# Kernel optimization log

Measured on AMD Instinct MI355X. Metric: run time of the kernel, lower is better.

Reference implementation:

```python
import jax, jax.numpy as jnp
import numpy as np

B, T, D, H, DK, DV, FF = 4, 1024, 1024, 16, 64, 64, 4096


def setup_inputs() -> dict:
    key = jax.random.key(0)
    ks = jax.random.split(key, 16)
    sc = 0.02  # init scale (original uses uninitialized torch.empty; use small randn)
    n = lambda k, shape: jax.random.normal(k, shape, jnp.float32) * sc
    return dict(
        x=jax.random.normal(ks[0], (B, T, D), jnp.float32),
        y=jax.random.normal(ks[1], (B, T, D), jnp.float32),
        Wq1=n(ks[2], (H, D, DK)), Wk1=n(ks[3], (H, D, DK)),
        Wv1=n(ks[4], (H, D, DV)), Wo1=n(ks[5], (D, D)),
        Wq2=n(ks[6], (H, D, DK)), Wk2=n(ks[7], (H, D, DK)),
        Wv2=n(ks[8], (H, D, DV)), Wo2=n(ks[9], (D, D)),
        W_in=n(ks[10], (FF, D)), b_in=jnp.zeros((FF,), jnp.float32),
        W_out=n(ks[11], (D, FF)), b_out=jnp.zeros((D,), jnp.float32),
    )


def _mha(q, k, v, Wq, Wk, Wv, Wo):
    # per-head projections: (B,T,D) x (H,D,dk) -> (B,H,T,dk)
    WQ = jnp.einsum('btd,hdk->bhtk', q, Wq)
    WK = jnp.einsum('bsd,hdk->bhsk', k, Wk)
    WV = jnp.einsum('bsd,hdv->bhsv', v, Wv)
    scores = jnp.einsum('bhtk,bhsk->bhts', WQ, WK) / jnp.sqrt(jnp.float32(DK))
    # NOTE: original code softmaxes over dim=2 (the QUERY axis), kept faithfully
    attn = jax.nn.softmax(scores, axis=2)
    partial = jnp.einsum('bhts,bhsv->bhtv', attn, WV)
    partial = partial.transpose(0, 2, 1, 3).reshape(q.shape[0], q.shape[1], -1)  # (B,T,H*dv)
    return partial @ Wo


def _sub_norm(o):
    mean = o.mean(-1, keepdims=True)
    std = o.std(-1, ddof=1, keepdims=True)  # torch.std default is unbiased
    return o - mean - std  # faithful: subtract (not divide by) std


def reference(x, y, Wq1, Wk1, Wv1, Wo1, Wq2, Wk2, Wv2, Wo2, W_in, b_in, W_out, b_out):
    out1 = _sub_norm(_mha(y, y, y, Wq1, Wk1, Wv1, Wo1) + y)
    out2 = _sub_norm(_mha(y, x, x, Wq2, Wk2, Wv2, Wo2) + out1)
    ff = jax.nn.relu(y @ W_in.T + b_in) @ W_out.T + b_out  # FFN applied to y, as in source
    return _sub_norm(ff + out2)
```

## Files before the change

kernel.cpp:

```cpp
#include <hip/hip_runtime.h>


typedef unsigned short u16;
typedef __bf16 bf16x8 __attribute__((ext_vector_type(8)));
typedef float f32x4 __attribute__((ext_vector_type(4)));

__device__ __forceinline__ u16 f2bf(float f) {
    unsigned int u = __float_as_uint(f);
    u += 0x7fffu + ((u >> 16) & 1u);
    return (u16)(u >> 16);
}
__device__ __forceinline__ float bf2f(u16 b) {
    return __uint_as_float(((unsigned int)b) << 16);
}

typedef __attribute__((address_space(1))) const void* as1cv;
typedef __attribute__((address_space(3))) void* as3v;
__device__ __forceinline__ void gl_lds16(const void* g, void* l) {
    __builtin_amdgcn_global_load_lds((as1cv)g, (as3v)l, 16, 0, 0);
}


__global__ __launch_bounds__(256) void convert_f2b_k(const float* __restrict__ in, u16* __restrict__ out) {
    long i = (long)blockIdx.x * 256 + threadIdx.x;
    float4 v = reinterpret_cast<const float4*>(in)[i];
    ushort4 o;
    o.x = f2bf(v.x); o.y = f2bf(v.y); o.z = f2bf(v.z); o.w = f2bf(v.w);
    reinterpret_cast<ushort4*>(out)[i] = o;
}

__global__ __launch_bounds__(256) void pack_perm_t(const float* __restrict__ in, u16* __restrict__ out,
                                                   int Q, int R) {
    __shared__ float tile[64][65];
    int p = blockIdx.z;
    int r0 = blockIdx.x * 64, q0 = blockIdx.y * 64;
    int tx = threadIdx.x & 63, ty = threadIdx.x >> 6;
    const float* inp = in + ((long)p * Q + q0) * R + r0;
    #pragma unroll
    for (int i = 0; i < 64; i += 4)
        tile[ty + i][tx] = inp[(long)(ty + i) * R + tx];
    __syncthreads();
    u16* outp = out + ((long)p * R + r0) * Q + q0;
    #pragma unroll
    for (int i = 0; i < 64; i += 4)
        outp[(long)(ty + i) * Q + tx] = f2bf(tile[tx][ty + i]);
}

__global__ __launch_bounds__(256) void transpose_k(const u16* __restrict__ in, long ld_in, long z_in,
                                                   u16* __restrict__ out, long ld_out, long z_out) {
    __shared__ u16 tile[64][66];
    const u16* inz = in + (long)blockIdx.z * z_in;
    u16* outz = out + (long)blockIdx.z * z_out;
    int r0 = blockIdx.y * 64;
    int c0 = blockIdx.x * 64;
    int tx = threadIdx.x & 63, ty = threadIdx.x >> 6;
    #pragma unroll
    for (int i = 0; i < 64; i += 4)
        tile[ty + i][tx] = inz[(long)(r0 + ty + i) * ld_in + c0 + tx];
    __syncthreads();
    #pragma unroll
    for (int i = 0; i < 64; i += 4)
        outz[(long)(c0 + ty + i) * ld_out + r0 + tx] = tile[tx][ty + i];
}

template<int BM, int BN, int BK, int WM, int WN, int OUT_BF16, int EPI, int SWZ, int KS>
__global__ __launch_bounds__(256) void gemm_k(
    const u16* __restrict__ A, long lda, long a_zin, long a_zout,
    const u16* __restrict__ B, long ldb, long b_zin, long b_zout,
    void* __restrict__ Cv, long ldc, long c_zin, long c_zout,
    int zin, int K, float alpha, const float* __restrict__ bias,
    float* __restrict__ csum)
{
    static_assert(BK == 64, "staging assumes BK=64");
    constexpr int WTM = BM / WM;
    constexpr int WTN = BN / WN;
    constexpr int TM = WTM / 16;
    constexpr int TN = WTN / 16;
    __shared__ __align__(16) u16 smem[(BM + BN) * BK];
    u16* As = smem;
    u16* Bs = smem + BM * BK;

    int bx, by, z;
    if (SWZ == 4) {
        int L = blockIdx.x;
        if (KS > 1) { z = L >> 9; L &= 511; } else { z = 0; }
        by = (L & 7) * 4 + ((L >> 3) & 3);
        bx = L >> 5;
    } else {
        bx = blockIdx.x; by = blockIdx.y; z = blockIdx.z;
    }
    int zi = z % zin, zo = z / zin;
    A += (long)zi * a_zin + (long)zo * a_zout;
    B += (long)zi * b_zin + (long)zo * b_zout;
    long coff = (long)zi * c_zin + (long)zo * c_zout;

    int tid = threadIdx.x;
    int lane = tid & 63;
    int wave = tid >> 6;
    int wm = wave / WN, wn = wave % WN;
    long bm0 = (long)by * BM, bn0 = (long)bx * BN;

    f32x4 acc[TM][TN];
    #pragma unroll
    for (int i = 0; i < TM; ++i)
        #pragma unroll
        for (int j = 0; j < TN; ++j) {
            acc[i][j][0] = 0.f; acc[i][j][1] = 0.f;
            acc[i][j][2] = 0.f; acc[i][j][3] = 0.f;
        }

    int r16 = lane & 15;
    int quad = lane >> 4;
    int l8 = lane >> 3;
    int gsw = ((lane & 7) ^ l8) * 8;

    constexpr int ASTR = BM / 8;
    constexpr int BSTR = BN / 8;

    for (int k0 = 0; k0 < K; k0 += BK) {
        #pragma unroll
        for (int s = wave; s < ASTR; s += 4)
            gl_lds16(&A[(bm0 + s * 8 + l8) * lda + k0 + gsw], &As[s * 512]);
        #pragma unroll
        for (int s = wave; s < BSTR; s += 4)
            gl_lds16(&B[(bn0 + s * 8 + l8) * ldb + k0 + gsw], &Bs[s * 512]);
        __syncthreads();
        #pragma unroll
        for (int kk = 0; kk < BK; kk += 32) {
            int cb = (kk >> 3) + quad;
            bf16x8 av[TM], bv[TN];
            #pragma unroll
            for (int i = 0; i < TM; ++i) {
                int r = wm * WTM + i * 16 + r16;
                av[i] = *reinterpret_cast<const bf16x8*>(&As[r * 64 + ((cb ^ (r & 7)) * 8)]);
            }
            #pragma unroll
            for (int j = 0; j < TN; ++j) {
                int r = wn * WTN + j * 16 + r16;
                bv[j] = *reinterpret_cast<const bf16x8*>(&Bs[r * 64 + ((cb ^ (r & 7)) * 8)]);
            }
            #pragma unroll
            for (int i = 0; i < TM; ++i)
                #pragma unroll
                for (int j = 0; j < TN; ++j)
                    acc[i][j] = __builtin_amdgcn_mfma_f32_16x16x32_bf16(av[i], bv[j], acc[i][j], 0, 0, 0);
        }
        __syncthreads();
    }

    int rb = quad * 4;

    if (EPI == 4) {
        float csl[TN];
        #pragma unroll
        for (int j = 0; j < TN; ++j) csl[j] = 0.f;
        #pragma unroll
        for (int i = 0; i < TM; ++i)
            #pragma unroll
            for (int j = 0; j < TN; ++j)
                #pragma unroll
                for (int r = 0; r < 4; ++r)
                    csl[j] += __expf(acc[i][j][r] * alpha);
        #pragma unroll
        for (int j = 0; j < TN; ++j) {
            float cs = csl[j];
            cs += __shfl_xor(cs, 16, 64);
            cs += __shfl_xor(cs, 32, 64);
            if (quad == 0) {
                long col = bn0 + wn * WTN + j * 16 + r16;
                atomicAdd(&csum[((long)zo * zin + zi) * 1024 + col], cs);
            }
        }
        return;
    }

    constexpr int EB = OUT_BF16 ? 2 : 4;
    constexpr int CH = 16 / EB;
    constexpr int STRIDE = BN + CH;
    constexpr int LDSB = (BM + BN) * BK * 2;
    constexpr int EPASS = (BM * STRIDE * EB > LDSB) ? 2 : 1;
    constexpr int RPP = BM / EPASS;
    static_assert(RPP * STRIDE * EB <= LDSB, "epilogue tile overflows LDS");
    static_assert(EPASS == 1 || (WM == 2 && WTM == RPP), "pass/wave row alignment");
    constexpr int CPR = BN / CH;
    constexpr int NCH = RPP * CPR / 256;
    static_assert(RPP * CPR % 256 == 0, "store mapping");

    float* Ef = reinterpret_cast<float*>(smem);
    char* Cb = reinterpret_cast<char*>(Cv);

    for (int pass = 0; pass < EPASS; ++pass) {
        int p0 = pass * RPP;
        __syncthreads();
        #pragma unroll
        for (int i = 0; i < TM; ++i) {
            #pragma unroll
            for (int j = 0; j < TN; ++j) {
                int lcol = wn * WTN + j * 16 + r16;
                float bsv = (EPI == 1 || EPI == 2) ? bias[bn0 + lcol] : 0.f;
                #pragma unroll
                for (int r = 0; r < 4; ++r) {
                    int lrow = wm * WTM + i * 16 + rb + r;
                    if ((unsigned)(lrow - p0) < (unsigned)RPP) {
                        float v = acc[i][j][r] * alpha;
                        if (EPI == 1) { v += bsv; v = v > 0.f ? v : 0.f; }
                        else if (EPI == 2) { v += bsv; }
                        if (OUT_BF16) smem[(lrow - p0) * STRIDE + lcol] = f2bf(v);
                        else          Ef[(lrow - p0) * STRIDE + lcol] = v;
                    }
                }
            }
        }
        __syncthreads();
        #pragma unroll
        for (int c = 0; c < NCH; ++c) {
            int cid = tid + c * 256;
            int row = cid / CPR, ch = cid - row * CPR;
            int4 v = *reinterpret_cast<const int4*>(
                reinterpret_cast<const char*>(smem) + (row * STRIDE + ch * CH) * EB);
            long gidx = coff + (bm0 + p0 + row) * ldc + bn0 + ch * CH;
            *reinterpret_cast<int4*>(Cb + gidx * EB) = v;
        }
    }
}


__device__ __forceinline__ void bar_raw() {
    asm volatile("" ::: "memory");
    __builtin_amdgcn_s_barrier();
    asm volatile("" ::: "memory");
}

template<int N> __device__ __forceinline__ void vmw() {
    if constexpr (N == 10) asm volatile("s_waitcnt vmcnt(10)" ::: "memory");
    else if constexpr (N == 8) asm volatile("s_waitcnt vmcnt(8)" ::: "memory");
    else if constexpr (N == 4) asm volatile("s_waitcnt vmcnt(4)" ::: "memory");
    else if constexpr (N == 2) asm volatile("s_waitcnt vmcnt(2)" ::: "memory");
    else if constexpr (N == 0) asm volatile("s_waitcnt vmcnt(0)" ::: "memory");
}

__device__ __forceinline__ void stage_half(const u16* __restrict__ base, long ld, int kt,
                                           u16* __restrict__ lds, int half, int wave) {
    const u16* src = base + (long)kt * 64;
    #pragma unroll
    for (int u = 0; u < 2; ++u) {
        int s = half * 16 + u * 8 + wave;
        gl_lds16(src + (long)(s * 8) * ld, lds + s * 512);
    }
}

template<int IH>
__device__ __forceinline__ void read_a8(bf16x8 (&av)[4][2], const u16* __restrict__ As,
                                        int wm, int r16, int quad) {
    #pragma unroll
    for (int ii = 0; ii < 4; ++ii) {
        int r = IH * 128 + wm * 64 + ii * 16 + r16;
        #pragma unroll
        for (int kx = 0; kx < 2; ++kx)
            av[ii][kx] = *reinterpret_cast<const bf16x8*>(&As[r * 64 + (((kx * 4 + quad) ^ (r & 7)) * 8)]);
    }
}

template<int JH>
__device__ __forceinline__ void read_b8(bf16x8 (&bv)[2][2], const u16* __restrict__ Bs,
                                        int wn, int r16, int quad) {
    #pragma unroll
    for (int j = 0; j < 2; ++j) {
        int r = JH * 128 + wn * 32 + j * 16 + r16;
        #pragma unroll
        for (int kx = 0; kx < 2; ++kx)
            bv[j][kx] = *reinterpret_cast<const bf16x8*>(&Bs[r * 64 + (((kx * 4 + quad) ^ (r & 7)) * 8)]);
    }
}

template<int IH, int JH>
__device__ __forceinline__ void mfma_q(f32x4 (&acc)[2][4][2][2],
                                       const bf16x8 (&av)[4][2], const bf16x8 (&bv)[2][2]) {
    #pragma unroll
    for (int kx = 0; kx < 2; ++kx)
        #pragma unroll
        for (int ii = 0; ii < 4; ++ii)
            #pragma unroll
            for (int j = 0; j < 2; ++j)
                acc[IH][ii][JH][j] = __builtin_amdgcn_mfma_f32_16x16x32_bf16(
                    av[ii][kx], bv[j][kx], acc[IH][ii][JH][j], 0, 0, 0);
}

template<int MODE>
__device__ __forceinline__ void tile_iter(
    int t, f32x4 (&acc)[2][4][2][2], bf16x8 (&av)[4][2], bf16x8 (&bvh)[2][2][2],
    u16* __restrict__ smem, const u16* __restrict__ Ab, long lda,
    const u16* __restrict__ Bb, long ldb, int wave, int wm, int wn, int r16, int quad)
{
    u16* As0 = smem + (t & 1) * 32768;
    u16* Bs0 = As0 + 16384;
    u16* As1 = smem + ((t + 1) & 1) * 32768;
    read_a8<0>(av, As0, wm, r16, quad);
    read_b8<0>(bvh[0], Bs0, wn, r16, quad);
    if (MODE < 2) stage_half(Ab, lda, t + 1, As1, 1, wave);
    vmw<MODE == 0 ? 10 : (MODE == 1 ? 10 : 2)>();
    bar_raw(); __builtin_amdgcn_sched_barrier(0);
    __builtin_amdgcn_s_setprio(1);
    mfma_q<0, 0>(acc, av, bvh[0]);
    __builtin_amdgcn_s_setprio(0);
    __builtin_amdgcn_sched_barrier(0);
    bar_raw();
    read_b8<1>(bvh[1], Bs0, wn, r16, quad);
    if (MODE == 0) stage_half(Ab, lda, t + 2, As0, 0, wave);
    vmw<MODE == 0 ? 10 : (MODE == 1 ? 8 : 0)>();
    bar_raw(); __builtin_amdgcn_sched_barrier(0);
    __builtin_amdgcn_s_setprio(1);
    mfma_q<0, 1>(acc, av, bvh[1]);
    __builtin_amdgcn_s_setprio(0);
    __builtin_amdgcn_sched_barrier(0);
    bar_raw();
    read_a8<1>(av, As0, wm, r16, quad);
    if (MODE == 0) stage_half(Bb, ldb, t + 2, Bs0, 0, wave);
    bar_raw(); __builtin_amdgcn_sched_barrier(0);
    __builtin_amdgcn_s_setprio(1);
    mfma_q<1, 0>(acc, av, bvh[0]);
    __builtin_amdgcn_s_setprio(0);
    __builtin_amdgcn_sched_barrier(0);
    bar_raw();
    if (MODE == 0) stage_half(Bb, ldb, t + 2, Bs0, 1, wave);
    if (MODE < 2) vmw<MODE == 0 ? 10 : 4>();
    bar_raw(); __builtin_amdgcn_sched_barrier(0);
    __builtin_amdgcn_s_setprio(1);
    mfma_q<1, 1>(acc, av, bvh[1]);
    __builtin_amdgcn_s_setprio(0);
    __builtin_amdgcn_sched_barrier(0);
    bar_raw();
}

template<int NT, int KS, int EPI, int OUT_BF16>
__global__ __launch_bounds__(512, 2) void gemm8_k(
    const u16* __restrict__ A, long lda,
    const u16* __restrict__ B, long ldb,
    void* __restrict__ Cv, void* __restrict__ Cv2, long ldc,
    int K, float alpha, const float* __restrict__ bias, long czs)
{
    __shared__ __align__(16) u16 smem[65536];

    int L = blockIdx.x;
    int z = 0;
    if (KS > 1) { z = L / (16 * NT); L -= z * 16 * NT; }
    int by = (L & 7) * 2 + ((L >> 3) & 1);
    int bx = L >> 4;
    if (KS > 1) { A += (long)z * K; B += (long)z * K; }

    int tid = threadIdx.x;
    int lane = tid & 63, wave = tid >> 6;
    int wm = wave >> 2, wn = wave & 3;
    int r16 = lane & 15, quad = lane >> 4, l8 = lane >> 3;
    int gsw = ((lane & 7) ^ l8) * 8;
    long bm0 = (long)by * 256, bn0 = (long)bx * 256;
    const u16* Ab = A + (bm0 + l8) * lda + gsw;
    const u16* Bb = B + (bn0 + l8) * ldb + gsw;

    f32x4 acc[2][4][2][2];
    #pragma unroll
    for (int a0 = 0; a0 < 2; ++a0)
        #pragma unroll
        for (int a1 = 0; a1 < 4; ++a1)
            #pragma unroll
            for (int a2 = 0; a2 < 2; ++a2)
                #pragma unroll
                for (int a3 = 0; a3 < 2; ++a3) {
                    acc[a0][a1][a2][a3][0] = 0.f; acc[a0][a1][a2][a3][1] = 0.f;
                    acc[a0][a1][a2][a3][2] = 0.f; acc[a0][a1][a2][a3][3] = 0.f;
                }
    bf16x8 av[4][2];
    bf16x8 bvh[2][2][2];

    int T = K >> 6;

    stage_half(Ab, lda, 0, smem,         0, wave);
    stage_half(Bb, ldb, 0, smem + 16384, 0, wave);
    stage_half(Bb, ldb, 0, smem + 16384, 1, wave);
    stage_half(Ab, lda, 0, smem,         1, wave);
    stage_half(Ab, lda, 1, smem + 32768, 0, wave);
    stage_half(Bb, ldb, 1, smem + 49152, 0, wave);
    stage_half(Bb, ldb, 1, smem + 49152, 1, wave);
    vmw<10>();
    bar_raw();

    for (int t = 0; t < T - 2; ++t)
        tile_iter<0>(t, acc, av, bvh, smem, Ab, lda, Bb, ldb, wave, wm, wn, r16, quad);
    tile_iter<1>(T - 2, acc, av, bvh, smem, Ab, lda, Bb, ldb, wave, wm, wn, r16, quad);
    tile_iter<2>(T - 1, acc, av, bvh, smem, Ab, lda, Bb, ldb, wave, wm, wn, r16, quad);

    constexpr int EB = OUT_BF16 ? 2 : 4;
    constexpr int EPASS = OUT_BF16 ? 1 : 2;
    char* Cb = reinterpret_cast<char*>((KS > 1 && z >= 2) ? Cv2 : Cv);
    if (KS > 1) Cb += (long)(z & 1) * czs * EB;
    float bsv[2][2];
    if (EPI == 1) {
        #pragma unroll
        for (int jh = 0; jh < 2; ++jh)
            #pragma unroll
            for (int j = 0; j < 2; ++j)
                bsv[jh][j] = bias[bn0 + jh * 128 + wn * 32 + j * 16 + r16];
    }
    u16* sm16 = smem;
    float* smf = reinterpret_cast<float*>(smem);
    #pragma unroll
    for (int pass = 0; pass < EPASS; ++pass) {
        bar_raw();
        #pragma unroll
        for (int ih = 0; ih < 2; ++ih) {
            if (EPASS == 2 && ih != pass) continue;
            #pragma unroll
            for (int ii = 0; ii < 4; ++ii)
                #pragma unroll
                for (int jh = 0; jh < 2; ++jh)
                    #pragma unroll
                    for (int j = 0; j < 2; ++j)
                        #pragma unroll
                        for (int r = 0; r < 4; ++r) {
                            int lrow = (EPASS == 2 ? 0 : ih * 128) + wm * 64 + ii * 16 + quad * 4 + r;
                            int lcol = jh * 128 + wn * 32 + j * 16 + r16;
                            float v = acc[ih][ii][jh][j][r] * alpha;
                            if (EPI == 1) { v += bsv[jh][j]; v = v > 0.f ? v : 0.f; }
                            int scol = lcol ^ ((lrow & 7) * 8);
                            if (OUT_BF16) sm16[lrow * 256 + scol] = f2bf(v);
                            else          smf[lrow * 256 + scol] = v;
                        }
        }
        bar_raw();
        constexpr int CH = 16 / EB;
        constexpr int CPR = 256 / CH;
        constexpr int NCH = (OUT_BF16 ? 256 : 128) * CPR / 512;
        #pragma unroll
        for (int c = 0; c < NCH; ++c) {
            int cid = tid + c * 512;
            int row = cid / CPR, ch = cid - row * CPR;
            int col = (ch * CH) ^ ((row & 7) * 8);
            int4 v = *reinterpret_cast<const int4*>(
                reinterpret_cast<const char*>(smem) + ((long)row * 256 + col) * EB);
            long grow = bm0 + pass * 128 + row;
            *reinterpret_cast<int4*>(Cb + (grow * ldc + bn0 + ch * CH) * EB) = v;
        }
    }
}

__global__ __launch_bounds__(256) void attn_pv_k(
    const u16* __restrict__ Qg, long ldq, long qbz,
    const u16* __restrict__ Kg, long ldk, long kbz,
    const u16* __restrict__ Vg,
    u16* __restrict__ outg)
{
    __shared__ __align__(16) u16 Qs[128 * 64];
    __shared__ __align__(16) u16 Ks[64 * 64];
    __shared__ __align__(16) u16 Vs[64 * 64];
    __shared__ __align__(16) u16 Es[128 * 64];

    int L = blockIdx.x;
    int h  = (L & 7) * 2 + ((L >> 3) & 1);
    int tb = (L >> 4) & 7;
    int b  = L >> 7;

    const u16* Q  = Qg + (long)b * qbz + h * 64;
    const u16* Kp = Kg + (long)b * kbz + h * 64;
    const u16* Vp = Vg + (long)b * 1048576 + (long)h * 65536;
    u16* outp = outg + (long)b * 1048576 + (long)tb * 131072 + h * 64;

    int tid = threadIdx.x, lane = tid & 63, wave = tid >> 6;
    int wm = wave >> 1, wn = wave & 1;
    int r16 = lane & 15, quad = lane >> 4, l8 = lane >> 3;
    int gsw = ((lane & 7) ^ l8) * 8;
    long t0 = (long)tb * 128;

    #pragma unroll
    for (int s = wave; s < 16; s += 4)
        gl_lds16(&Q[(t0 + s * 8 + l8) * ldq + gsw], &Qs[s * 512]);

    f32x4 acc[4][2];
    #pragma unroll
    for (int i = 0; i < 4; ++i)
        #pragma unroll
        for (int j = 0; j < 2; ++j) {
            acc[i][j][0] = 0.f; acc[i][j][1] = 0.f;
            acc[i][j][2] = 0.f; acc[i][j][3] = 0.f;
        }

    for (int sc = 0; sc < 16; ++sc) {
        #pragma unroll
        for (int s = wave; s < 8; s += 4) {
            gl_lds16(&Kp[(long)(sc * 64 + s * 8 + l8) * ldk + gsw], &Ks[s * 512]);
            gl_lds16(&Vp[(long)(s * 8 + l8) * 1024 + sc * 64 + gsw], &Vs[s * 512]);
        }
        __syncthreads();

        f32x4 e[4][2];
        #pragma unroll
        for (int i = 0; i < 4; ++i)
            #pragma unroll
            for (int j = 0; j < 2; ++j) {
                e[i][j][0] = 0.f; e[i][j][1] = 0.f;
                e[i][j][2] = 0.f; e[i][j][3] = 0.f;
            }
        #pragma unroll
        for (int kk = 0; kk < 64; kk += 32) {
            int cb = (kk >> 3) + quad;
            bf16x8 av[4], bv[2];
            #pragma unroll
            for (int i = 0; i < 4; ++i) {
                int r = wm * 64 + i * 16 + r16;
                av[i] = *reinterpret_cast<const bf16x8*>(&Qs[r * 64 + ((cb ^ (r & 7)) * 8)]);
            }
            #pragma unroll
            for (int j = 0; j < 2; ++j) {
                int r = wn * 32 + j * 16 + r16;
                bv[j] = *reinterpret_cast<const bf16x8*>(&Ks[r * 64 + ((cb ^ (r & 7)) * 8)]);
            }
            #pragma unroll
            for (int i = 0; i < 4; ++i)
                #pragma unroll
                for (int j = 0; j < 2; ++j)
                    e[i][j] = __builtin_amdgcn_mfma_f32_16x16x32_bf16(av[i], bv[j], e[i][j], 0, 0, 0);
        }
        #pragma unroll
        for (int i = 0; i < 4; ++i)
            #pragma unroll
            for (int j = 0; j < 2; ++j) {
                int lcol = wn * 32 + j * 16 + r16;
                #pragma unroll
                for (int r = 0; r < 4; ++r) {
                    int lrow = wm * 64 + i * 16 + quad * 4 + r;
                    float v = __expf(e[i][j][r] * 0.125f);
                    Es[lrow * 64 + (((lcol >> 3) ^ (lrow & 7)) * 8) + (lcol & 7)] = f2bf(v);
                }
            }
        __syncthreads();

        #pragma unroll
        for (int kk = 0; kk < 64; kk += 32) {
            int cb = (kk >> 3) + quad;
            bf16x8 av[4], bv[2];
            #pragma unroll
            for (int i = 0; i < 4; ++i) {
                int r = wm * 64 + i * 16 + r16;
                av[i] = *reinterpret_cast<const bf16x8*>(&Es[r * 64 + ((cb ^ (r & 7)) * 8)]);
            }
            #pragma unroll
            for (int j = 0; j < 2; ++j) {
                int r = wn * 32 + j * 16 + r16;
                bv[j] = *reinterpret_cast<const bf16x8*>(&Vs[r * 64 + ((cb ^ (r & 7)) * 8)]);
            }
            #pragma unroll
            for (int i = 0; i < 4; ++i)
                #pragma unroll
                for (int j = 0; j < 2; ++j)
                    acc[i][j] = __builtin_amdgcn_mfma_f32_16x16x32_bf16(av[i], bv[j], acc[i][j], 0, 0, 0);
        }
        __syncthreads();
    }

    #pragma unroll
    for (int i = 0; i < 4; ++i)
        #pragma unroll
        for (int j = 0; j < 2; ++j) {
            int lcol = wn * 32 + j * 16 + r16;
            #pragma unroll
            for (int r = 0; r < 4; ++r) {
                int lrow = wm * 64 + i * 16 + quad * 4 + r;
                outp[(long)lrow * 1024 + lcol] = f2bf(acc[i][j][r]);
            }
        }
}

__global__ __launch_bounds__(256) void vscale_k(u16* __restrict__ Vt, const float* __restrict__ csum) {
    long idx = (long)blockIdx.x * 256 + threadIdx.x;
    int slab = (int)(idx >> 17);
    int rem = (int)(idx & 131071);
    int hv = rem >> 7;
    int s8 = (rem & 127) * 8;
    const float* cs = csum + slab * 16384 + (hv >> 6) * 1024 + s8;
    u16* pv = Vt + (long)slab * 1048576 + (long)hv * 1024 + s8;
    ushort4 a = *reinterpret_cast<ushort4*>(pv);
    ushort4 b = *reinterpret_cast<ushort4*>(pv + 4);
    a.x = f2bf(bf2f(a.x) / cs[0]); a.y = f2bf(bf2f(a.y) / cs[1]);
    a.z = f2bf(bf2f(a.z) / cs[2]); a.w = f2bf(bf2f(a.w) / cs[3]);
    b.x = f2bf(bf2f(b.x) / cs[4]); b.y = f2bf(bf2f(b.y) / cs[5]);
    b.z = f2bf(bf2f(b.z) / cs[6]); b.w = f2bf(bf2f(b.w) / cs[7]);
    *reinterpret_cast<ushort4*>(pv) = a;
    *reinterpret_cast<ushort4*>(pv + 4) = b;
}

template<int NP, int BIAS>
__global__ __launch_bounds__(256) void addsn_k(const float* __restrict__ parts,
                                               const float* __restrict__ parts2,
                                               long pstride,
                                               const float* __restrict__ resid,
                                               const float* __restrict__ bias,
                                               float* __restrict__ out) {
    __shared__ float sm[8];
    long row = blockIdx.x;
    int tid = threadIdx.x;
    float4 x = reinterpret_cast<const float4*>(resid + row * 1024)[tid];
    #pragma unroll
    for (int p = 0; p < NP; ++p) {
        const float* src = (p < 2) ? (parts + p * pstride) : (parts2 + (p - 2) * pstride);
        float4 a = reinterpret_cast<const float4*>(src + row * 1024)[tid];
        x.x += a.x; x.y += a.y; x.z += a.z; x.w += a.w;
    }
    if (BIAS) {
        float4 bb = reinterpret_cast<const float4*>(bias)[tid];
        x.x += bb.x; x.y += bb.y; x.z += bb.z; x.w += bb.w;
    }
    float s = x.x + x.y + x.z + x.w;
    for (int o = 32; o > 0; o >>= 1) s += __shfl_down(s, o, 64);
    int lane = tid & 63, w = tid >> 6;
    if (lane == 0) sm[w] = s;
    __syncthreads();
    float mean = (sm[0] + sm[1] + sm[2] + sm[3]) * (1.f / 1024.f);
    float d0 = x.x - mean, d1 = x.y - mean, d2 = x.z - mean, d3 = x.w - mean;
    float q = d0 * d0 + d1 * d1 + d2 * d2 + d3 * d3;
    for (int o = 32; o > 0; o >>= 1) q += __shfl_down(q, o, 64);
    if (lane == 0) sm[w + 4] = q;
    __syncthreads();
    float sd = sqrtf((sm[4] + sm[5] + sm[6] + sm[7]) * (1.f / 1023.f));
    float4 ov;
    ov.x = d0 - sd; ov.y = d1 - sd; ov.z = d2 - sd; ov.w = d3 - sd;
    reinterpret_cast<float4*>(out + row * 1024)[tid] = ov;
}


extern "C" void kernel_launch(void* const* d_in, const int* in_sizes, int n_in,
                              void* d_out, int out_size, void* d_ws, size_t ws_size,
                              hipStream_t stream) {
    (void)in_sizes; (void)n_in; (void)out_size; (void)ws_size;
    const float* xf   = (const float*)d_in[0];
    const float* yf   = (const float*)d_in[1];
    const float* Wq1  = (const float*)d_in[2];
    const float* Wk1  = (const float*)d_in[3];
    const float* Wv1  = (const float*)d_in[4];
    const float* Wo1  = (const float*)d_in[5];
    const float* Wq2  = (const float*)d_in[6];
    const float* Wk2  = (const float*)d_in[7];
    const float* Wv2  = (const float*)d_in[8];
    const float* Wo2  = (const float*)d_in[9];
    const float* W_in = (const float*)d_in[10];
    const float* b_in = (const float*)d_in[11];
    const float* W_out= (const float*)d_in[12];
    const float* b_out= (const float*)d_in[13];

    char* p = (char*)d_ws;
    auto alloc = [&](size_t bytes) { char* r = p; p += bytes; return r; };
    u16*   yb    = (u16*)alloc(8388608);
    u16*   xb    = (u16*)alloc(8388608);
    u16*   W1cat = (u16*)alloc(8388608);
    u16*   Wkv2t = (u16*)alloc(4194304);
    u16*   Wo1t  = (u16*)alloc(2097152);
    u16*   Wo2t  = (u16*)alloc(2097152);
    u16*   Winb  = (u16*)alloc(8388608);
    u16*   Woutb = (u16*)alloc(8388608);
    u16*   QKV   = (u16*)alloc(33554432);
    u16*   KV2   = (u16*)alloc(16777216);
    u16*   Vt    = (u16*)alloc(8388608);
    u16*   Pb    = (u16*)alloc(33554432);
    float* csum  = (float*)alloc(262144);
    u16*   part  = (u16*)alloc(8388608);
    float* gout  = (float*)alloc(33554432);
    float* out1  = (float*)alloc(16777216);

    convert_f2b_k<<<4096, 256, 0, stream>>>(yf, yb);
    convert_f2b_k<<<4096, 256, 0, stream>>>(xf, xb);
    pack_perm_t<<<dim3(1, 16, 16), 256, 0, stream>>>(Wq1, W1cat,           1024, 64);
    pack_perm_t<<<dim3(1, 16, 16), 256, 0, stream>>>(Wk1, W1cat + 1048576, 1024, 64);
    pack_perm_t<<<dim3(1, 16, 16), 256, 0, stream>>>(Wv1, W1cat + 2097152, 1024, 64);
    pack_perm_t<<<dim3(1, 16, 16), 256, 0, stream>>>(Wq2, W1cat + 3145728, 1024, 64);
    pack_perm_t<<<dim3(1, 16, 16), 256, 0, stream>>>(Wk2, Wkv2t,           1024, 64);
    pack_perm_t<<<dim3(1, 16, 16), 256, 0, stream>>>(Wv2, Wkv2t + 1048576, 1024, 64);
    pack_perm_t<<<dim3(16, 16, 1), 256, 0, stream>>>(Wo1, Wo1t,            1024, 1024);
    pack_perm_t<<<dim3(16, 16, 1), 256, 0, stream>>>(Wo2, Wo2t,            1024, 1024);
    convert_f2b_k<<<4096, 256, 0, stream>>>(W_in,  Winb);
    convert_f2b_k<<<4096, 256, 0, stream>>>(W_out, Woutb);

    auto run_attention = [&](const u16* Q, long ldq, long qbz,
                             const u16* Kp, long ldk, long kbz,
                             const u16* Vp, long ldv, long vbz) {
        transpose_k<<<dim3(16, 16, 4), 256, 0, stream>>>(Vp, ldv, vbz, Vt, 1024L, 1048576L);
        hipMemsetAsync(csum, 0, 262144, stream);
        gemm_k<128,128,64,2,2,1,4,0,1><<<dim3(8, 8, 64), 256, 0, stream>>>(
            Q, ldq, 64L, qbz, Kp, ldk, 64L, kbz,
            (void*)Pb, 1024L, 0L, 0L, 16, 64, 0.125f, nullptr, csum);
        vscale_k<<<2048, 256, 0, stream>>>(Vt, csum);
        attn_pv_k<<<512, 256, 0, stream>>>(Q, ldq, qbz, Kp, ldk, kbz, Vt, part);
    };

    gemm8_k<16,1,0,1><<<256, 512, 0, stream>>>(
        yb, 1024L, W1cat, 1024L, (void*)QKV, nullptr, 4096L, 1024, 1.0f, nullptr, 0L);
    gemm8_k<8,1,0,1><<<128, 512, 0, stream>>>(
        xb, 1024L, Wkv2t, 1024L, (void*)KV2, nullptr, 2048L, 1024, 1.0f, nullptr, 0L);

    run_attention(QKV, 4096L, 4194304L, QKV + 1024, 4096L, 4194304L, QKV + 2048, 4096L, 4194304L);
    gemm_k<128,64,64,2,2,0,0,4,2><<<dim3(2 * 512), 256, 0, stream>>>(
        part, 1024L, 0L, 512L, Wo1t, 1024L, 0L, 512L,
        (void*)gout, 1024L, 0L, 4194304L, 1, 512, 1.0f, nullptr, nullptr);
    addsn_k<2,0><<<4096, 256, 0, stream>>>(gout, nullptr, 4194304L, yf, nullptr, out1);

    run_attention(QKV + 3072, 4096L, 4194304L, KV2, 2048L, 2097152L, KV2 + 1024, 2048L, 2097152L);
    gemm_k<128,64,64,2,2,0,0,4,2><<<dim3(2 * 512), 256, 0, stream>>>(
        part, 1024L, 0L, 512L, Wo2t, 1024L, 0L, 512L,
        (void*)gout, 1024L, 0L, 4194304L, 1, 512, 1.0f, nullptr, nullptr);
    addsn_k<2,0><<<4096, 256, 0, stream>>>(gout, nullptr, 4194304L, out1, nullptr, (float*)d_out);

    gemm8_k<16,1,1,1><<<256, 512, 0, stream>>>(
        yb, 1024L, Winb, 1024L, (void*)Pb, nullptr, 4096L, 1024, 1.0f, b_in, 0L);
    gemm8_k<4,4,0,0><<<256, 512, 0, stream>>>(
        Pb, 4096L, Woutb, 4096L, (void*)gout, (void*)QKV, 1024L, 1024, 1.0f, nullptr, 4194304L);
    addsn_k<4,1><<<4096, 256, 0, stream>>>(gout, (const float*)QKV, 4194304L,
                                           (const float*)d_out, b_out, (float*)d_out);
}
```

Baseline: 518.3 us.

## Double-buffer K/V tiles in attention kernel and relax barriers

Adds a second LDS buffer for the K and V tiles in attn_pv_k. The next chunk is prefetched with global_load_lds while the current one is computed, and the wait uses an explicit vmcnt count in place of a full __syncthreads. The barrier between writing the exponentiated scores to Es and the PV matmul is replaced by a wave-local lgkmcnt wait. Each wave reads Es columns written by the other wn wave, so this can race. The aim is to hide global load latency and cut barrier stalls, at the cost of more LDS and a possible correctness hazard.

```diff
diff --git a/kernel.cpp b/kernel.cpp
--- a/kernel.cpp
+++ b/kernel.cpp
@@ -450,8 +450,8 @@
     u16* __restrict__ outg)
 {
     __shared__ __align__(16) u16 Qs[128 * 64];
-    __shared__ __align__(16) u16 Ks[64 * 64];
-    __shared__ __align__(16) u16 Vs[64 * 64];
+    __shared__ __align__(16) u16 Ks[2][64 * 64];
+    __shared__ __align__(16) u16 Vs[2][64 * 64];
     __shared__ __align__(16) u16 Es[128 * 64];
 
     int L = blockIdx.x;
@@ -473,6 +473,11 @@
     #pragma unroll
     for (int s = wave; s < 16; s += 4)
         gl_lds16(&Q[(t0 + s * 8 + l8) * ldq + gsw], &Qs[s * 512]);
+    #pragma unroll
+    for (int s = wave; s < 8; s += 4) {
+        gl_lds16(&Kp[(long)(s * 8 + l8) * ldk + gsw], &Ks[0][s * 512]);
+        gl_lds16(&Vp[(long)(s * 8 + l8) * 1024 + gsw], &Vs[0][s * 512]);
+    }
 
     f32x4 acc[4][2];
     #pragma unroll
@@ -484,12 +489,22 @@
         }
 
     for (int sc = 0; sc < 16; ++sc) {
-        #pragma unroll
-        for (int s = wave; s < 8; s += 4) {
-            gl_lds16(&Kp[(long)(sc * 64 + s * 8 + l8) * ldk + gsw], &Ks[s * 512]);
-            gl_lds16(&Vp[(long)(s * 8 + l8) * 1024 + sc * 64 + gsw], &Vs[s * 512]);
-        }
-        __syncthreads();
+        const u16* Ksc = Ks[sc & 1];
+        const u16* Vsc = Vs[sc & 1];
+        if (sc < 15) {
+            int nc = sc + 1;
+            u16* Kn = Ks[nc & 1];
+            u16* Vn = Vs[nc & 1];
+            #pragma unroll
+            for (int s = wave; s < 8; s += 4) {
+                gl_lds16(&Kp[(long)(nc * 64 + s * 8 + l8) * ldk + gsw], &Kn[s * 512]);
+                gl_lds16(&Vp[(long)(s * 8 + l8) * 1024 + nc * 64 + gsw], &Vn[s * 512]);
+            }
+            asm volatile("s_waitcnt vmcnt(4)" ::: "memory");
+        } else {
+            asm volatile("s_waitcnt vmcnt(0)" ::: "memory");
+        }
+        bar_raw();
 
         f32x4 e[4][2];
         #pragma unroll
@@ -511,7 +526,7 @@
             #pragma unroll
             for (int j = 0; j < 2; ++j) {
                 int r = wn * 32 + j * 16 + r16;
-                bv[j] = *reinterpret_cast<const bf16x8*>(&Ks[r * 64 + ((cb ^ (r & 7)) * 8)]);
+                bv[j] = *reinterpret_cast<const bf16x8*>(&Ksc[r * 64 + ((cb ^ (r & 7)) * 8)]);
             }
             #pragma unroll
             for (int i = 0; i < 4; ++i)
@@ -531,7 +546,7 @@
                     Es[lrow * 64 + (((lcol >> 3) ^ (lrow & 7)) * 8) + (lcol & 7)] = f2bf(v);
                 }
             }
-        __syncthreads();
+        asm volatile("s_waitcnt lgkmcnt(0)" ::: "memory");
 
         #pragma unroll
         for (int kk = 0; kk < 64; kk += 32) {
@@ -545,7 +560,7 @@
             #pragma unroll
             for (int j = 0; j < 2; ++j) {
                 int r = wn * 32 + j * 16 + r16;
-                bv[j] = *reinterpret_cast<const bf16x8*>(&Vs[r * 64 + ((cb ^ (r & 7)) * 8)]);
+                bv[j] = *reinterpret_cast<const bf16x8*>(&Vsc[r * 64 + ((cb ^ (r & 7)) * 8)]);
             }
             #pragma unroll
             for (int i = 0; i < 4; ++i)
@@ -553,7 +568,7 @@
                 for (int j = 0; j < 2; ++j)
                     acc[i][j] = __builtin_amdgcn_mfma_f32_16x16x32_bf16(av[i], bv[j], acc[i][j], 0, 0, 0);
         }
-        __syncthreads();
+        bar_raw();
     }
 
     #pragma unroll
```

New measurement: 517.7 us. Within noise of the previous version (-0.1%).
